# Kernel optimization log

Measured on AMD Instinct MI355X. Metric: run time of the kernel, lower is better.

The kernel has to match this reference:

```python
import jax, jax.numpy as jnp
import numpy as np

B, S, D_MODEL = 2, 2048, 2048
H, DS, DG, DV = 16, 64, 64, 128
ROPE_BASE = 10000.0
NEG_INF = -1e9


def _rope(x, base=ROPE_BASE):
    # x: [B, S, H, D] -> rotate-half RoPE over positions 0..S-1
    d = x.shape[-1]
    half = d // 2
    inv_freq = 1.0 / (base ** (jnp.arange(half, dtype=jnp.float32) / half))
    ang = jnp.arange(x.shape[1], dtype=jnp.float32)[:, None] * inv_freq  # [S, half]
    cos = jnp.cos(ang)[None, :, None, :]
    sin = jnp.sin(ang)[None, :, None, :]
    x1, x2 = x[..., :half], x[..., half:]
    return jnp.concatenate([x1 * cos - x2 * sin, x1 * sin + x2 * cos], axis=-1)


def setup_inputs() -> dict:
    key = jax.random.key(0)
    ks = jax.random.split(key, 8)
    s = lambda fan_in: 1.0 / np.sqrt(fan_in)
    return {
        "x": jax.random.normal(ks[0], (B, S, D_MODEL), dtype=jnp.float32),
        "wq_sem": jax.random.normal(ks[1], (D_MODEL, H * DS), dtype=jnp.float32) * s(D_MODEL),
        "wk_sem": jax.random.normal(ks[2], (D_MODEL, H * DS), dtype=jnp.float32) * s(D_MODEL),
        "wq_geo": jax.random.normal(ks[3], (D_MODEL, H * DG), dtype=jnp.float32) * s(D_MODEL),
        "wk_geo": jax.random.normal(ks[4], (D_MODEL, H * DG), dtype=jnp.float32) * s(D_MODEL),
        "wv": jax.random.normal(ks[5], (D_MODEL, H * DV), dtype=jnp.float32) * s(D_MODEL),
        "wo": jax.random.normal(ks[6], (H * DV, D_MODEL), dtype=jnp.float32) * s(H * DV),
        "gate_logit": jax.random.normal(ks[7], (H,), dtype=jnp.float32),
    }


def reference(x, wq_sem, wk_sem, wq_geo, wk_geo, wv, wo, gate_logit):
    b, sl, _ = x.shape
    # Projections -> [B, S, H, d]
    qs = (x @ wq_sem).reshape(b, sl, H, DS)
    ksem = (x @ wk_sem).reshape(b, sl, H, DS)
    qg = _rope((x @ wq_geo).reshape(b, sl, H, DG))
    kg = _rope((x @ wk_geo).reshape(b, sl, H, DG))
    v = (x @ wv).reshape(b, sl, H, DV)

    sem_scale = 1.0 / np.sqrt(DS)
    geo_scale = 1.0 / np.sqrt(DG)
    sem_scores = jnp.einsum("bqhd,bkhd->bhqk", qs, ksem) * sem_scale
    geo_scores = jnp.einsum("bqhd,bkhd->bhqk", qg, kg) * geo_scale

    # Learned per-head gate mixing semantic vs geometric paths
    g = jax.nn.sigmoid(gate_logit)[None, :, None, None]
    scores = g * sem_scores + (1.0 - g) * geo_scores

    causal = jnp.tril(jnp.ones((sl, sl), dtype=bool))
    scores = jnp.where(causal[None, None], scores, NEG_INF)
    attn = jax.nn.softmax(scores, axis=-1)

    out = jnp.einsum("bhqk,bkhd->bqhd", attn, v).reshape(b, sl, H * DV)
    return out @ wo
```

## Files before the change

### kernel.cpp

```cpp
#include <hip/hip_runtime.h>
#include <hip/hip_bf16.h>

typedef unsigned short u16;
typedef __attribute__((ext_vector_type(4))) float floatx4;
typedef __attribute__((ext_vector_type(8))) __bf16 bf16x8;

__device__ __forceinline__ u16 f2bf(float f) {
  unsigned int x = __builtin_bit_cast(unsigned int, f);
  unsigned int r = (x + 0x7fffu + ((x >> 16) & 1u)) >> 16;
  return (u16)r;
}
__device__ __forceinline__ float bf2f(u16 u) {
  unsigned int x = ((unsigned int)u) << 16;
  return __builtin_bit_cast(float, x);
}
__device__ __forceinline__ floatx4 mfma16(bf16x8 a, bf16x8 b, floatx4 c) {
  return __builtin_amdgcn_mfma_f32_16x16x32_bf16(a, b, c, 0, 0, 0);
}
__device__ __forceinline__ void gload16(const u16* g, u16* l) {
  __builtin_amdgcn_global_load_lds(
      (const __attribute__((address_space(1))) unsigned int*)g,
      (__attribute__((address_space(3))) unsigned int*)l, 16, 0, 0);
}
#define SCHEDB() __builtin_amdgcn_sched_barrier(0)
#define SBAR() __builtin_amdgcn_s_barrier()

#define BB 2
#define SS 2048
#define DM 2048
#define HH 16
#define PCOLS 6144

__global__ void convert_bf16_k(const float* __restrict__ src, u16* __restrict__ dst, size_t n) {
  size_t i = ((size_t)blockIdx.x * blockDim.x + threadIdx.x) * 4;
  if (i + 3 >= n) { for (size_t j = i; j < n; ++j) dst[j] = f2bf(src[j]); return; }
  float4 v = *(const float4*)&src[i];
  ushort4 o; o.x = f2bf(v.x); o.y = f2bf(v.y); o.z = f2bf(v.z); o.w = f2bf(v.w);
  *(ushort4*)&dst[i] = o;
}

__global__ void transpose_all_k(const float* w0, const float* w1, const float* w2,
                                const float* w3, const float* w4, const float* w5,
                                u16* __restrict__ WcatT, u16* __restrict__ WoT) {
  __shared__ float tile[32][33];
  const int z = blockIdx.z;
  const float* src; u16* dst; int cols;
  if (z == 0)      { src = w0; dst = WcatT;                        cols = 1024; }
  else if (z == 1) { src = w1; dst = WcatT + (size_t)1024 * 2048;  cols = 1024; }
  else if (z == 2) { src = w2; dst = WcatT + (size_t)2048 * 2048;  cols = 1024; }
  else if (z == 3) { src = w3; dst = WcatT + (size_t)3072 * 2048;  cols = 1024; }
  else if (z == 4) { src = w4; dst = WcatT + (size_t)4096 * 2048;  cols = 2048; }
  else             { src = w5; dst = WoT;                          cols = 2048; }
  int c0 = blockIdx.x * 32;
  if (c0 >= cols) return;
  int r0 = blockIdx.y * 32;
  int tx = threadIdx.x, ty = threadIdx.y;
#pragma unroll
  for (int i = 0; i < 4; ++i)
    tile[ty + i * 8][tx] = src[(size_t)(r0 + ty + i * 8) * cols + c0 + tx];
  __syncthreads();
#pragma unroll
  for (int i = 0; i < 4; ++i)
    dst[(size_t)(c0 + ty + i * 8) * 2048 + r0 + tx] = f2bf(tile[tx][ty + i * 8]);
}

__global__ void vtrans_k(const u16* __restrict__ P, u16* __restrict__ VtG) {
  __shared__ u16 t[32][33];
  int b = blockIdx.z;
  int c0 = blockIdx.x * 32;
  int s0 = blockIdx.y * 32;
  int tx = threadIdx.x, ty = threadIdx.y;
#pragma unroll
  for (int i = 0; i < 4; ++i)
    t[ty + i * 8][tx] = P[((size_t)b * SS + s0 + ty + i * 8) * PCOLS + 4096 + c0 + tx];
  __syncthreads();
#pragma unroll
  for (int i = 0; i < 4; ++i)
    VtG[((size_t)b * 2048 + c0 + ty + i * 8) * SS + s0 + tx] = t[tx][ty + i * 8];
}

__global__ void rope_table_k(float* __restrict__ cosT, float* __restrict__ sinT) {
  int idx = blockIdx.x * 256 + threadIdx.x;
  int s = idx >> 5, d = idx & 31;
  double inv = pow(10000.0, -(double)d / 32.0);
  double ang = (double)s * inv;
  cosT[idx] = (float)cos(ang);
  sinT[idx] = (float)sin(ang);
}

__global__ void rope_apply_k(u16* __restrict__ P, const float* __restrict__ cosT,
                             const float* __restrict__ sinT) {
  int idx = blockIdx.x * 256 + threadIdx.x;
  int d = idx & 31, h = (idx >> 5) & 15, reg = (idx >> 9) & 1, row = idx >> 10;
  int s = row & (SS - 1);
  size_t base = (size_t)row * PCOLS + (reg ? 3072 : 2048) + h * 64 + d;
  float x1 = bf2f(P[base]), x2 = bf2f(P[base + 32]);
  float c = cosT[s * 32 + d], sn = sinT[s * 32 + d];
  P[base] = f2bf(x1 * c - x2 * sn);
  P[base + 32] = f2bf(x1 * sn + x2 * c);
}

template <bool OUTF32>
__global__ __launch_bounds__(512, 1)
void gemm2p_k(const u16* __restrict__ A, const u16* __restrict__ Bt,
              void* __restrict__ Cout, int M, int N, int K) {
  __shared__ alignas(16) u16 lds[49152];
  const int tid = threadIdx.x;
  const int wid = tid >> 6, lane = tid & 63;
  const int lr = lane & 15, lg = lane >> 4;
  const int wr = wid >> 2, wc = wid & 3;
  const int m0 = blockIdx.y * 128, n0 = blockIdx.x * 256;
  const int NT = K >> 6;

  const int aoff = lr * 32 + ((lg ^ ((lr >> 1) & 3)) * 8);

  const int srow = tid >> 2;
  const int sgl = (((tid & 3) ^ ((tid >> 3) & 3)) * 8);
  const u16* Asrc = A + (size_t)(m0 + srow) * K + sgl;
  const u16* Bsrc = Bt + (size_t)(n0 + srow) * K + sgl;

  floatx4 acc[4][4];
#pragma unroll
  for (int m = 0; m < 4; ++m)
#pragma unroll
    for (int n = 0; n < 4; ++n) acc[m][n] = (floatx4){0.f, 0.f, 0.f, 0.f};

  auto stage_tile = [&](int tile) {
    if (tile >= NT) return;
    const int buf = tile & 1;
#pragma unroll
    for (int kh = 0; kh < 2; ++kh) {
      const int rb = buf * 2 + kh;
      gload16(Asrc + tile * 64 + kh * 32, lds + rb * 4096 + wid * 512);
      u16* db = lds + 16384 + rb * 8192 + wid * 512;
      const u16* sb = Bsrc + tile * 64 + kh * 32;
      gload16(sb, db);
      gload16(sb + (size_t)128 * K, db + 4096);
    }
  };

  stage_tile(0);
  asm volatile("s_waitcnt vmcnt(0)" ::: "memory");
  SCHEDB(); SBAR(); SCHEDB();

#pragma unroll 1
  for (int t = 0; t < NT; ++t) {
    const int buf = t & 1;
    const u16* A0 = lds + (buf * 2 + 0) * 4096;
    const u16* A1 = lds + (buf * 2 + 1) * 4096;
    const u16* B0 = lds + 16384 + (buf * 2 + 0) * 8192;
    const u16* B1 = lds + 16384 + (buf * 2 + 1) * 8192;

    stage_tile(t + 1);
    asm volatile("s_waitcnt vmcnt(6)" ::: "memory");
    SCHEDB(); SBAR(); SCHEDB();

    bf16x8 af0[4], bf0v[4], af1[4], bf1v[4];
#pragma unroll
    for (int m = 0; m < 4; ++m)
      af0[m] = *(const bf16x8*)&A0[(wr * 64 + m * 16) * 32 + aoff];
#pragma unroll
    for (int n = 0; n < 4; ++n)
      bf0v[n] = *(const bf16x8*)&B0[(wc * 64 + n * 16) * 32 + aoff];
#pragma unroll
    for (int m = 0; m < 4; ++m)
      af1[m] = *(const bf16x8*)&A1[(wr * 64 + m * 16) * 32 + aoff];
#pragma unroll
    for (int n = 0; n < 4; ++n)
      bf1v[n] = *(const bf16x8*)&B1[(wc * 64 + n * 16) * 32 + aoff];

    __builtin_amdgcn_s_setprio(1);
#pragma unroll
    for (int m = 0; m < 4; ++m)
#pragma unroll
      for (int n = 0; n < 4; ++n)
        acc[m][n] = mfma16(af0[m], bf0v[n], acc[m][n]);
#pragma unroll
    for (int m = 0; m < 4; ++m)
#pragma unroll
      for (int n = 0; n < 4; ++n)
        acc[m][n] = mfma16(af1[m], bf1v[n], acc[m][n]);
    __builtin_amdgcn_s_setprio(0);
    SCHEDB(); SBAR(); SCHEDB();
  }

#pragma unroll
  for (int m = 0; m < 4; ++m) {
    int row0 = m0 + wr * 64 + m * 16 + lg * 4;
#pragma unroll
    for (int n = 0; n < 4; ++n) {
      int col = n0 + wc * 64 + n * 16 + lr;
#pragma unroll
      for (int r = 0; r < 4; ++r) {
        size_t off = (size_t)(row0 + r) * N + col;
        if (OUTF32) ((float*)Cout)[off] = acc[m][n][r];
        else        ((u16*)Cout)[off] = f2bf(acc[m][n][r]);
      }
    }
  }
}

__device__ __forceinline__ bf16x8 load_scaled(const u16* p, float s) {
  uint4 raw = *(const uint4*)p;
  const u16* ru = (const u16*)&raw;
  bf16x8 out;
#pragma unroll
  for (int j = 0; j < 8; ++j) out[j] = (__bf16)(bf2f(ru[j]) * s);
  return out;
}

__global__ __launch_bounds__(256, 3)
void attn_k(const u16* __restrict__ P, const u16* __restrict__ VtG,
            const float* __restrict__ gate, u16* __restrict__ AttO) {
  const int pairi = blockIdx.x >> 4;
  const int h = blockIdx.x & 15;
  const int b = blockIdx.y;
  const int tid = threadIdx.x, wid = tid >> 6, lane = tid & 63;
  const int lr = lane & 15, lg = lane >> 4;
  const size_t rowb = (size_t)b * SS;

  const float g = 1.f / (1.f + __expf(-gate[h]));
  const float ssc = g * 0.125f;
  const float gsc = (1.f - g) * 0.125f;

  __shared__ alignas(16) u16 Ks[64 * 64];
  __shared__ alignas(16) u16 Kg[64 * 64];
  __shared__ alignas(16) u16 Vt[128 * 64];
  __shared__ alignas(16) u16 Pw[4][16 * 64];

  const int strow = tid >> 3;
  const int stg = ((tid & 7) ^ (strow & 7)) * 8;
  const int swz = lr & 7;

  for (int half = 0; half < 2; ++half) {
    const int qb = half ? (31 - pairi) : pairi;
    const int q0 = qb * 64;

    const u16* qbase = P + (rowb + q0 + wid * 16 + lr) * PCOLS + h * 64;
    bf16x8 qs[2], qg[2];
#pragma unroll
    for (int kk = 0; kk < 2; ++kk) {
      qs[kk] = load_scaled(qbase + kk * 32 + lg * 8, ssc);
      qg[kk] = load_scaled(qbase + 2048 + kk * 32 + lg * 8, gsc);
    }

    float m_r = -1e30f, l_r = 0.f;
    floatx4 o[8];
#pragma unroll
    for (int n = 0; n < 8; ++n) o[n] = (floatx4){0.f, 0.f, 0.f, 0.f};

    const int nkv = q0 + 64;
    for (int kv0 = 0; kv0 < nkv; kv0 += 64) {
      __syncthreads();
      {
        const u16* ks = P + (rowb + kv0 + strow) * PCOLS + 1024 + h * 64 + stg;
        const u16* gs = P + (rowb + kv0 + strow) * PCOLS + 3072 + h * 64 + stg;
        gload16(ks, Ks + wid * 512);
        gload16(gs, Kg + wid * 512);
        gload16(ks + (size_t)32 * PCOLS, Ks + 2048 + wid * 512);
        gload16(gs + (size_t)32 * PCOLS, Kg + 2048 + wid * 512);
      }
      {
        const u16* vs = VtG + ((size_t)b * 2048 + h * 128 + strow) * SS + kv0 + stg;
#pragma unroll
        for (int c = 0; c < 4; ++c)
          gload16(vs + (size_t)(c * 32) * SS, Vt + c * 2048 + wid * 512);
      }
      __syncthreads();

      floatx4 sc[4];
#pragma unroll
      for (int s = 0; s < 4; ++s) sc[s] = (floatx4){0.f, 0.f, 0.f, 0.f};
#pragma unroll
      for (int kk = 0; kk < 2; ++kk) {
#pragma unroll
        for (int s = 0; s < 4; ++s) {
          bf16x8 kf = *(const bf16x8*)&Ks[(s * 16 + lr) * 64 + ((kk * 4 + lg) ^ swz) * 8];
          bf16x8 gf = *(const bf16x8*)&Kg[(s * 16 + lr) * 64 + ((kk * 4 + lg) ^ swz) * 8];
          sc[s] = mfma16(kf, qs[kk], sc[s]);
          sc[s] = mfma16(gf, qg[kk], sc[s]);
        }
      }

      const int qrow = q0 + wid * 16 + lr;
      const bool needmask = (kv0 + 63 > q0 + wid * 16);
      float vv[4][4];
      float vmax = -1e30f;
#pragma unroll
      for (int s = 0; s < 4; ++s)
#pragma unroll
        for (int r = 0; r < 4; ++r) {
          float val = sc[s][r];
          if (needmask) val = (kv0 + s * 16 + lg * 4 + r <= qrow) ? val : -1e30f;
          vv[s][r] = val;
          vmax = fmaxf(vmax, val);
        }
      vmax = fmaxf(vmax, __shfl_xor(vmax, 16));
      vmax = fmaxf(vmax, __shfl_xor(vmax, 32));
      float mnew = fmaxf(m_r, vmax);
      float corr = __expf(m_r - mnew);
      float psum = 0.f;
#pragma unroll
      for (int s = 0; s < 4; ++s)
#pragma unroll
        for (int r = 0; r < 4; ++r) {
          vv[s][r] = __expf(vv[s][r] - mnew);
          psum += vv[s][r];
        }
      psum += __shfl_xor(psum, 16);
      psum += __shfl_xor(psum, 32);
      l_r = l_r * corr + psum;
      m_r = mnew;

#pragma unroll
      for (int s = 0; s < 4; ++s)
#pragma unroll
        for (int t = 0; t < 2; ++t) {
          unsigned int w;
          asm("v_cvt_pk_bf16_f32 %0, %1, %2" : "=v"(w) : "v"(vv[s][2 * t]), "v"(vv[s][2 * t + 1]));
          int u16off = lr * 64 + ((s * 2 + (lg >> 1)) ^ swz) * 8 + (lg & 1) * 4 + t * 2;
          *(unsigned int*)&Pw[wid][u16off] = w;
        }

      float crr[4];
#pragma unroll
      for (int r = 0; r < 4; ++r) crr[r] = __shfl(corr, lg * 4 + r);
#pragma unroll
      for (int n = 0; n < 8; ++n)
#pragma unroll
        for (int r = 0; r < 4; ++r) o[n][r] *= crr[r];

      asm volatile("s_waitcnt lgkmcnt(0)" ::: "memory");
      SCHEDB();
      bf16x8 pa0 = *(const bf16x8*)&Pw[wid][lr * 64 + (lg ^ swz) * 8];
      bf16x8 pa1 = *(const bf16x8*)&Pw[wid][lr * 64 + ((4 + lg) ^ swz) * 8];
#pragma unroll
      for (int n = 0; n < 8; ++n) {
        bf16x8 vb0 = *(const bf16x8*)&Vt[(n * 16 + lr) * 64 + (lg ^ swz) * 8];
        bf16x8 vb1 = *(const bf16x8*)&Vt[(n * 16 + lr) * 64 + ((4 + lg) ^ swz) * 8];
        o[n] = mfma16(pa0, vb0, o[n]);
        o[n] = mfma16(pa1, vb1, o[n]);
      }
    }

    float linv = 1.f / l_r;
    float lnv[4];
#pragma unroll
    for (int r = 0; r < 4; ++r) lnv[r] = __shfl(linv, lg * 4 + r);
#pragma unroll
    for (int n = 0; n < 8; ++n)
#pragma unroll
      for (int r = 0; r < 4; ++r) {
        float val = o[n][r] * lnv[r];
        AttO[(rowb + q0 + wid * 16 + lg * 4 + r) * (size_t)(HH * 128) + h * 128 + n * 16 + lr] =
            f2bf(val);
      }
  }
}

extern "C" void kernel_launch(void* const* d_in, const int* in_sizes, int n_in,
                              void* d_out, int out_size, void* d_ws, size_t ws_size,
                              hipStream_t stream) {
  const float* x       = (const float*)d_in[0];
  const float* wq_sem  = (const float*)d_in[1];
  const float* wk_sem  = (const float*)d_in[2];
  const float* wq_geo  = (const float*)d_in[3];
  const float* wk_geo  = (const float*)d_in[4];
  const float* wv      = (const float*)d_in[5];
  const float* wo      = (const float*)d_in[6];
  const float* gate    = (const float*)d_in[7];

  char* ws = (char*)d_ws;
  u16* Xbf   = (u16*)(ws);
  u16* WcatT = (u16*)(ws + 16777216);
  u16* WoT   = (u16*)(ws + 16777216 + 25165824);
  u16* P     = (u16*)(ws + 16777216 + 25165824 + 8388608);
  float* cosT = (float*)(ws + 16777216 + 25165824 + 8388608 + 50331648);
  float* sinT = cosT + 2048 * 32;
  u16* AttO = Xbf;
  u16* VtG  = WcatT;

  dim3 tb(32, 8);
  convert_bf16_k<<<8192, 256, 0, stream>>>(x, Xbf, (size_t)4096 * 2048);
  transpose_all_k<<<dim3(64, 64, 6), tb, 0, stream>>>(wq_sem, wk_sem, wq_geo, wk_geo,
                                                      wv, wo, WcatT, WoT);
  rope_table_k<<<256, 256, 0, stream>>>(cosT, sinT);

  gemm2p_k<false><<<dim3(24, 32), 512, 0, stream>>>(Xbf, WcatT, P, 4096, 6144, 2048);
  rope_apply_k<<<16384, 256, 0, stream>>>(P, cosT, sinT);
  vtrans_k<<<dim3(64, 64, 2), tb, 0, stream>>>(P, VtG);
  attn_k<<<dim3(256, 2), 256, 0, stream>>>(P, VtG, gate, AttO);
  gemm2p_k<true><<<dim3(8, 32), 512, 0, stream>>>(AttO, WoT, d_out, 4096, 2048, 2048);
}
```

Measured before the change: 284.1 us.

## Triple-buffer GEMM K-tiles with register prefetch and double-buffer attention KV loads

The GEMM moves from double to triple LDS buffering (144 KB shared memory). It stages tiles two ahead and preloads the first k-half fragments into registers, so LDS reads overlap MFMA work. The attention kernel double-buffers the K/Kg/Vt tiles, prefetching the next KV block while computing the current one, and lowers the launch-bounds occupancy hint from 3 to 2 to fit the doubled LDS. The cost is fewer resident blocks and careful vmcnt accounting, which risks subtle hazards.

```diff
diff --git a/kernel.cpp b/kernel.cpp
--- a/kernel.cpp
+++ b/kernel.cpp
@@ -102,9 +102,9 @@
 
 template <bool OUTF32>
 __global__ __launch_bounds__(512, 1)
-void gemm2p_k(const u16* __restrict__ A, const u16* __restrict__ Bt,
+void gemm3p_k(const u16* __restrict__ A, const u16* __restrict__ Bt,
               void* __restrict__ Cout, int M, int N, int K) {
-  __shared__ alignas(16) u16 lds[49152];
+  __shared__ alignas(16) u16 lds[73728];
   const int tid = threadIdx.x;
   const int wid = tid >> 6, lane = tid & 63;
   const int lr = lane & 15, lg = lane >> 4;
@@ -125,63 +125,68 @@
 #pragma unroll
     for (int n = 0; n < 4; ++n) acc[m][n] = (floatx4){0.f, 0.f, 0.f, 0.f};
 
-  auto stage_tile = [&](int tile) {
-    if (tile >= NT) return;
-    const int buf = tile & 1;
+  auto stage_tile = [&](int t) {
+    if (t >= NT) return;
+    const int b = t % 3;
+    u16* Ad = lds + b * 8192;
+    u16* Bd = lds + 24576 + b * 16384;
 #pragma unroll
     for (int kh = 0; kh < 2; ++kh) {
-      const int rb = buf * 2 + kh;
-      gload16(Asrc + tile * 64 + kh * 32, lds + rb * 4096 + wid * 512);
-      u16* db = lds + 16384 + rb * 8192 + wid * 512;
-      const u16* sb = Bsrc + tile * 64 + kh * 32;
-      gload16(sb, db);
-      gload16(sb + (size_t)128 * K, db + 4096);
+      gload16(Asrc + t * 64 + kh * 32, Ad + kh * 4096 + wid * 512);
+      const u16* sb = Bsrc + t * 64 + kh * 32;
+      gload16(sb, Bd + kh * 8192 + wid * 512);
+      gload16(sb + (size_t)128 * K, Bd + kh * 8192 + 4096 + wid * 512);
     }
   };
 
+  bf16x8 afA[4], bvA[4], afB[4], bvB[4];
+
+  auto rdA = [&](bf16x8* af, int t, int kh) {
+    const u16* Ab = lds + (t % 3) * 8192 + kh * 4096;
+#pragma unroll
+    for (int m = 0; m < 4; ++m)
+      af[m] = *(const bf16x8*)&Ab[(wr * 64 + m * 16) * 32 + aoff];
+  };
+  auto rdB = [&](bf16x8* bv, int t, int kh) {
+    const u16* Bb = lds + 24576 + (t % 3) * 16384 + kh * 8192;
+#pragma unroll
+    for (int n = 0; n < 4; ++n)
+      bv[n] = *(const bf16x8*)&Bb[(wc * 64 + n * 16) * 32 + aoff];
+  };
+
   stage_tile(0);
-  asm volatile("s_waitcnt vmcnt(0)" ::: "memory");
+  stage_tile(1);
+  asm volatile("s_waitcnt vmcnt(6)" ::: "memory");
   SCHEDB(); SBAR(); SCHEDB();
+  rdA(afA, 0, 0); rdB(bvA, 0, 0);
 
 #pragma unroll 1
   for (int t = 0; t < NT; ++t) {
-    const int buf = t & 1;
-    const u16* A0 = lds + (buf * 2 + 0) * 4096;
-    const u16* A1 = lds + (buf * 2 + 1) * 4096;
-    const u16* B0 = lds + 16384 + (buf * 2 + 0) * 8192;
-    const u16* B1 = lds + 16384 + (buf * 2 + 1) * 8192;
-
-    stage_tile(t + 1);
-    asm volatile("s_waitcnt vmcnt(6)" ::: "memory");
     SCHEDB(); SBAR(); SCHEDB();
-
-    bf16x8 af0[4], bf0v[4], af1[4], bf1v[4];
+    stage_tile(t + 2);
+    SCHEDB();
+    rdA(afB, t, 1); rdB(bvB, t, 1);
+    SCHEDB();
+    __builtin_amdgcn_s_setprio(1);
 #pragma unroll
     for (int m = 0; m < 4; ++m)
-      af0[m] = *(const bf16x8*)&A0[(wr * 64 + m * 16) * 32 + aoff];
-#pragma unroll
-    for (int n = 0; n < 4; ++n)
-      bf0v[n] = *(const bf16x8*)&B0[(wc * 64 + n * 16) * 32 + aoff];
+#pragma unroll
+      for (int n = 0; n < 4; ++n)
+        acc[m][n] = mfma16(afA[m], bvA[n], acc[m][n]);
+    __builtin_amdgcn_s_setprio(0);
+    SCHEDB();
+    if (t + 2 < NT) asm volatile("s_waitcnt vmcnt(6)" ::: "memory");
+    else            asm volatile("s_waitcnt vmcnt(0)" ::: "memory");
+    SCHEDB(); SBAR(); SCHEDB();
+    if (t + 1 < NT) { rdA(afA, t + 1, 0); rdB(bvA, t + 1, 0); }
+    SCHEDB();
+    __builtin_amdgcn_s_setprio(1);
 #pragma unroll
     for (int m = 0; m < 4; ++m)
-      af1[m] = *(const bf16x8*)&A1[(wr * 64 + m * 16) * 32 + aoff];
-#pragma unroll
-    for (int n = 0; n < 4; ++n)
-      bf1v[n] = *(const bf16x8*)&B1[(wc * 64 + n * 16) * 32 + aoff];
-
-    __builtin_amdgcn_s_setprio(1);
-#pragma unroll
-    for (int m = 0; m < 4; ++m)
 #pragma unroll
       for (int n = 0; n < 4; ++n)
-        acc[m][n] = mfma16(af0[m], bf0v[n], acc[m][n]);
-#pragma unroll
-    for (int m = 0; m < 4; ++m)
-#pragma unroll
-      for (int n = 0; n < 4; ++n)
-        acc[m][n] = mfma16(af1[m], bf1v[n], acc[m][n]);
+        acc[m][n] = mfma16(afB[m], bvB[n], acc[m][n]);
     __builtin_amdgcn_s_setprio(0);
-    SCHEDB(); SBAR(); SCHEDB();
   }
 
 #pragma unroll
@@ -209,7 +214,7 @@
   return out;
 }
 
-__global__ __launch_bounds__(256, 3)
+__global__ __launch_bounds__(256, 2)
 void attn_k(const u16* __restrict__ P, const u16* __restrict__ VtG,
             const float* __restrict__ gate, u16* __restrict__ AttO) {
   const int pairi = blockIdx.x >> 4;
@@ -223,14 +228,27 @@
   const float ssc = g * 0.125f;
   const float gsc = (1.f - g) * 0.125f;
 
-  __shared__ alignas(16) u16 Ks[64 * 64];
-  __shared__ alignas(16) u16 Kg[64 * 64];
-  __shared__ alignas(16) u16 Vt[128 * 64];
+  __shared__ alignas(16) u16 Ks[2][64 * 64];
+  __shared__ alignas(16) u16 Kg[2][64 * 64];
+  __shared__ alignas(16) u16 Vt[2][128 * 64];
   __shared__ alignas(16) u16 Pw[4][16 * 64];
 
   const int strow = tid >> 3;
   const int stg = ((tid & 7) ^ (strow & 7)) * 8;
   const int swz = lr & 7;
+
+  auto stageKV = [&](int kv0, int buf) {
+    const u16* ks = P + (rowb + kv0 + strow) * PCOLS + 1024 + h * 64 + stg;
+    const u16* gs = P + (rowb + kv0 + strow) * PCOLS + 3072 + h * 64 + stg;
+    gload16(ks, &Ks[buf][wid * 512]);
+    gload16(gs, &Kg[buf][wid * 512]);
+    gload16(ks + (size_t)32 * PCOLS, &Ks[buf][2048 + wid * 512]);
+    gload16(gs + (size_t)32 * PCOLS, &Kg[buf][2048 + wid * 512]);
+    const u16* vs = VtG + ((size_t)b * 2048 + h * 128 + strow) * SS + kv0 + stg;
+#pragma unroll
+    for (int c = 0; c < 4; ++c)
+      gload16(vs + (size_t)(c * 32) * SS, &Vt[buf][c * 2048 + wid * 512]);
+  };
 
   for (int half = 0; half < 2; ++half) {
     const int qb = half ? (31 - pairi) : pairi;
@@ -250,23 +268,20 @@
     for (int n = 0; n < 8; ++n) o[n] = (floatx4){0.f, 0.f, 0.f, 0.f};
 
     const int nkv = q0 + 64;
+
+    stageKV(0, 0);
+    asm volatile("s_waitcnt vmcnt(0)" ::: "memory");
+    SCHEDB(); SBAR(); SCHEDB();
+
     for (int kv0 = 0; kv0 < nkv; kv0 += 64) {
-      __syncthreads();
-      {
-        const u16* ks = P + (rowb + kv0 + strow) * PCOLS + 1024 + h * 64 + stg;
-        const u16* gs = P + (rowb + kv0 + strow) * PCOLS + 3072 + h * 64 + stg;
-        gload16(ks, Ks + wid * 512);
-        gload16(gs, Kg + wid * 512);
-        gload16(ks + (size_t)32 * PCOLS, Ks + 2048 + wid * 512);
-        gload16(gs + (size_t)32 * PCOLS, Kg + 2048 + wid * 512);
-      }
-      {
-        const u16* vs = VtG + ((size_t)b * 2048 + h * 128 + strow) * SS + kv0 + stg;
-#pragma unroll
-        for (int c = 0; c < 4; ++c)
-          gload16(vs + (size_t)(c * 32) * SS, Vt + c * 2048 + wid * 512);
-      }
-      __syncthreads();
+      const int cur = (kv0 >> 6) & 1;
+      const bool more = (kv0 + 64 < nkv);
+
+      if (more) stageKV(kv0 + 64, cur ^ 1);
+      SCHEDB();
+      if (more) asm volatile("s_waitcnt vmcnt(8)" ::: "memory");
+      else      asm volatile("s_waitcnt vmcnt(0)" ::: "memory");
+      SCHEDB(); SBAR(); SCHEDB();
 
       floatx4 sc[4];
 #pragma unroll
@@ -275,8 +290,8 @@
       for (int kk = 0; kk < 2; ++kk) {
 #pragma unroll
         for (int s = 0; s < 4; ++s) {
-          bf16x8 kf = *(const bf16x8*)&Ks[(s * 16 + lr) * 64 + ((kk * 4 + lg) ^ swz) * 8];
-          bf16x8 gf = *(const bf16x8*)&Kg[(s * 16 + lr) * 64 + ((kk * 4 + lg) ^ swz) * 8];
+          bf16x8 kf = *(const bf16x8*)&Ks[cur][(s * 16 + lr) * 64 + ((kk * 4 + lg) ^ swz) * 8];
+          bf16x8 gf = *(const bf16x8*)&Kg[cur][(s * 16 + lr) * 64 + ((kk * 4 + lg) ^ swz) * 8];
           sc[s] = mfma16(kf, qs[kk], sc[s]);
           sc[s] = mfma16(gf, qg[kk], sc[s]);
         }
@@ -336,11 +351,12 @@
       bf16x8 pa1 = *(const bf16x8*)&Pw[wid][lr * 64 + ((4 + lg) ^ swz) * 8];
 #pragma unroll
       for (int n = 0; n < 8; ++n) {
-        bf16x8 vb0 = *(const bf16x8*)&Vt[(n * 16 + lr) * 64 + (lg ^ swz) * 8];
-        bf16x8 vb1 = *(const bf16x8*)&Vt[(n * 16 + lr) * 64 + ((4 + lg) ^ swz) * 8];
+        bf16x8 vb0 = *(const bf16x8*)&Vt[cur][(n * 16 + lr) * 64 + (lg ^ swz) * 8];
+        bf16x8 vb1 = *(const bf16x8*)&Vt[cur][(n * 16 + lr) * 64 + ((4 + lg) ^ swz) * 8];
         o[n] = mfma16(pa0, vb0, o[n]);
         o[n] = mfma16(pa1, vb1, o[n]);
       }
+      SCHEDB(); SBAR(); SCHEDB();
     }
 
     float linv = 1.f / l_r;
@@ -386,9 +402,9 @@
                                                       wv, wo, WcatT, WoT);
   rope_table_k<<<256, 256, 0, stream>>>(cosT, sinT);
 
-  gemm2p_k<false><<<dim3(24, 32), 512, 0, stream>>>(Xbf, WcatT, P, 4096, 6144, 2048);
+  gemm3p_k<false><<<dim3(24, 32), 512, 0, stream>>>(Xbf, WcatT, P, 4096, 6144, 2048);
   rope_apply_k<<<16384, 256, 0, stream>>>(P, cosT, sinT);
   vtrans_k<<<dim3(64, 64, 2), tb, 0, stream>>>(P, VtG);
   attn_k<<<dim3(256, 2), 256, 0, stream>>>(P, VtG, gate, AttO);
-  gemm2p_k<true><<<dim3(8, 32), 512, 0, stream>>>(AttO, WoT, d_out, 4096, 2048, 2048);
-}
+  gemm3p_k<true><<<dim3(8, 32), 512, 0, stream>>>(AttO, WoT, d_out, 4096, 2048, 2048);
+}
```

Result: no change. 283.9 us (-0.1%).
